# Kernel tuning notes

Measured on AMD Instinct MI355X. Metric: run time of the kernel, lower is better.

The kernel has to match this reference:

```python
import jax, jax.numpy as jnp
import numpy as np
import math

D_MODEL = 1024
NHEAD = 16
D_K = D_MODEL // NHEAD
B, S = 2, 2048


def setup_inputs() -> dict:
    key = jax.random.key(0)
    ks = jax.random.split(key, 9)
    x = jax.random.normal(ks[0], (B, S, D_MODEL), dtype=jnp.float32)
    # causal mask, broadcastable to (B, nhead, S, S); 0 entries are masked out
    mask = jnp.tril(jnp.ones((S, S), dtype=jnp.int32))[None, None, :, :]
    scale = 1.0 / math.sqrt(D_MODEL)
    def lin(kw, kb):
        W = jax.random.uniform(kw, (D_MODEL, D_MODEL), dtype=jnp.float32, minval=-scale, maxval=scale)
        b = jax.random.uniform(kb, (D_MODEL,), dtype=jnp.float32, minval=-scale, maxval=scale)
        return W, b
    Wq, bq = lin(ks[1], ks[2])
    Wk, bk = lin(ks[3], ks[4])
    Wv, bv = lin(ks[5], ks[6])
    Wo, bo = lin(ks[7], ks[8])
    return {"x": x, "mask": mask, "Wq": Wq, "bq": bq, "Wk": Wk, "bk": bk,
            "Wv": Wv, "bv": bv, "Wo": Wo, "bo": bo}


def reference(x, mask, Wq, bq, Wk, bk, Wv, bv, Wo, bo):
    b, s, _ = x.shape
    def heads(W, bias):
        # (b, s, d_model) @ (d_model, d_model) -> (b, nhead, s, d_k)
        return (x @ W.T + bias).reshape(b, s, NHEAD, D_K).transpose(0, 2, 1, 3)
    Q, K, V = heads(Wq, bq), heads(Wk, bk), heads(Wv, bv)
    scores = jnp.einsum('bhqd,bhkd->bhqk', Q, K) / math.sqrt(D_K)
    scores = jnp.where(mask == 0, jnp.float32(-1e9), scores)
    attn = jax.nn.softmax(scores, axis=-1)  # dropout is identity in eval mode
    out = jnp.einsum('bhqk,bhkd->bhqd', attn, V)
    out = out.transpose(0, 2, 1, 3).reshape(b, s, D_MODEL)
    return out @ Wo.T + bo
```

## Files before the change

### kernel.cpp

```cpp
#include <hip/hip_runtime.h>
#include <hip/hip_bf16.h>

#define DMODEL 1024
#define NH     16
#define DKH    64
#define BSZ    2
#define SEQ    2048
#define MROWS  (BSZ*SEQ)
#define WELEM  (DMODEL*DMODEL)

typedef __attribute__((ext_vector_type(8))) short short8;
typedef __attribute__((ext_vector_type(4))) short short4v;
typedef __attribute__((ext_vector_type(4))) float f32x4;

__device__ __forceinline__ f32x4 mfma_pv16(short4v a, short4v b, f32x4 c) {
#if defined(__HIP_DEVICE_COMPILE__)
#if __has_builtin(__builtin_amdgcn_mfma_f32_16x16x16bf16_1k)
    return __builtin_amdgcn_mfma_f32_16x16x16bf16_1k(a, b, c, 0, 0, 0);
#elif __has_builtin(__builtin_amdgcn_mfma_f32_16x16x16_bf16)
    return __builtin_amdgcn_mfma_f32_16x16x16_bf16(a, b, c, 0, 0, 0);
#else
    f32x4 d;
    asm volatile("v_mfma_f32_16x16x16_bf16 %0, %1, %2, %3"
                 : "=v"(d) : "v"(a), "v"(b), "v"(c));
    return d;
#endif
#else
    (void)a; (void)b;
    return c;
#endif
}

__device__ __forceinline__ ushort f2bf(float f) {
    return __bfloat16_as_ushort(__float2bfloat16(f));
}
__device__ __forceinline__ unsigned pk2(float lo, float hi) {
    return (unsigned)f2bf(lo) | ((unsigned)f2bf(hi) << 16);
}
__device__ __forceinline__ void load_lds16(const ushort* g, ushort* l) {
    __builtin_amdgcn_global_load_lds(
        (const __attribute__((address_space(1))) unsigned int*)g,
        (__attribute__((address_space(3))) unsigned int*)l, 16, 0, 0);
}

__global__ __launch_bounds__(256)
void cvt_all(const float* __restrict__ x,
             const float* __restrict__ W0, const float* __restrict__ W1,
             const float* __restrict__ W2, const float* __restrict__ W3,
             ushort* __restrict__ xbf, ushort* __restrict__ Wcat,
             ushort* __restrict__ Wo)
{
    const int blk = blockIdx.x;
    const float* src;
    ushort* dst;
    int base;
    if (blk < 2048)      { src = x;  dst = xbf;             base = blk * 2048; }
    else if (blk < 2560) { src = W0; dst = Wcat;            base = (blk - 2048) * 2048; }
    else if (blk < 3072) { src = W1; dst = Wcat + WELEM;    base = (blk - 2560) * 2048; }
    else if (blk < 3584) { src = W2; dst = Wcat + 2*WELEM;  base = (blk - 3072) * 2048; }
    else                 { src = W3; dst = Wo;              base = (blk - 3584) * 2048; }
    const size_t off = (size_t)base + threadIdx.x * 8;
    const float4 f0 = *(const float4*)(src + off);
    const float4 f1 = *(const float4*)(src + off + 4);
    uint4 o;
    o.x = pk2(f0.x, f0.y); o.y = pk2(f0.z, f0.w);
    o.z = pk2(f1.x, f1.y); o.w = pk2(f1.z, f1.w);
    *(uint4*)(dst + off) = o;
}

__global__ __launch_bounds__(256)
void gemm_qkv(const ushort* __restrict__ xbf, const ushort* __restrict__ Wcat,
              const float* __restrict__ bq, const float* __restrict__ bk,
              const float* __restrict__ bv,
              ushort* __restrict__ Qh, ushort* __restrict__ Kh,
              ushort* __restrict__ VT)
{
    __shared__ ushort Ash[128][32];
    __shared__ ushort Bsh[128][32];

    const int t    = threadIdx.x;
    const int m0   = blockIdx.y * 128, n0 = blockIdx.x * 128;
    const int wave = t >> 6;
    const int lane = t & 63;
    const int wr   = (wave >> 1) * 64;
    const int wc   = (wave & 1) * 64;
    const int quad = lane >> 4;
    const int r16  = lane & 15;

    const int row0 = wave * 16 + (lane >> 2);
    const int row1 = 64 + wave * 16 + (lane >> 2);
    const int ch   = (lane & 3) * 8;

    f32x4 acc[4][4];
    #pragma unroll
    for (int i = 0; i < 4; ++i)
        #pragma unroll
        for (int j = 0; j < 4; ++j)
            acc[i][j] = (f32x4){0.f, 0.f, 0.f, 0.f};

    for (int k0 = 0; k0 < DMODEL; k0 += 32) {
        load_lds16(xbf  + (size_t)(m0 + row0) * DMODEL + k0 + ch, &Ash[wave * 16][0]);
        load_lds16(xbf  + (size_t)(m0 + row1) * DMODEL + k0 + ch, &Ash[64 + wave * 16][0]);
        load_lds16(Wcat + (size_t)(n0 + row0) * DMODEL + k0 + ch, &Bsh[wave * 16][0]);
        load_lds16(Wcat + (size_t)(n0 + row1) * DMODEL + k0 + ch, &Bsh[64 + wave * 16][0]);
        __syncthreads();

        short8 af[4], bf[4];
        #pragma unroll
        for (int i = 0; i < 4; ++i) af[i] = *(const short8*)&Ash[wr + i * 16 + r16][quad * 8];
        #pragma unroll
        for (int j = 0; j < 4; ++j) bf[j] = *(const short8*)&Bsh[wc + j * 16 + r16][quad * 8];

        #pragma unroll
        for (int i = 0; i < 4; ++i)
            #pragma unroll
            for (int j = 0; j < 4; ++j)
                acc[i][j] = __builtin_amdgcn_mfma_f32_16x16x32_bf16(af[i], bf[j], acc[i][j], 0, 0, 0);
        __syncthreads();
    }

    const int region = n0 >> 10;
    const float* bp  = (region == 0) ? bq : (region == 1) ? bk : bv;
    ushort* outQK    = (region == 0) ? Qh : Kh;
    const float osc  = (region == 0) ? 0.18033688f : 1.0f;
    const int nbase  = n0 & 1023;

    #pragma unroll
    for (int i = 0; i < 4; ++i) {
        #pragma unroll
        for (int j = 0; j < 4; ++j) {
            #pragma unroll
            for (int reg = 0; reg < 4; ++reg) {
                const int m  = m0 + wr + i * 16 + quad * 4 + reg;
                const int n  = nbase + wc + j * 16 + r16;
                const float v = (acc[i][j][reg] + bp[n]) * osc;
                const int b = m >> 11, s = m & (SEQ - 1);
                const int h = n >> 6,  dk = n & 63;
                if (region < 2) {
                    outQK[((size_t)(b * NH + h) * SEQ + s) * DKH + dk] = f2bf(v);
                } else {
                    VT[(((size_t)(b * NH + h)) * DKH + dk) * SEQ + s] = f2bf(v);
                }
            }
        }
    }
}

__global__ __launch_bounds__(256)
void gemm_out(const ushort* __restrict__ O, const ushort* __restrict__ Wo,
              const float* __restrict__ bo, float* __restrict__ out)
{
    __shared__ ushort Ash[128][32];
    __shared__ ushort Bsh[64][32];

    const int t    = threadIdx.x;
    const int m0   = blockIdx.y * 128, n0 = blockIdx.x * 64;
    const int wave = t >> 6;
    const int lane = t & 63;
    const int wr   = (wave >> 1) * 64;
    const int wc   = (wave & 1) * 32;
    const int quad = lane >> 4;
    const int r16  = lane & 15;

    const int row0 = wave * 16 + (lane >> 2);
    const int row1 = 64 + wave * 16 + (lane >> 2);
    const int ch   = (lane & 3) * 8;

    f32x4 acc[4][2];
    #pragma unroll
    for (int i = 0; i < 4; ++i)
        #pragma unroll
        for (int j = 0; j < 2; ++j)
            acc[i][j] = (f32x4){0.f, 0.f, 0.f, 0.f};

    for (int k0 = 0; k0 < DMODEL; k0 += 32) {
        const int ma0 = m0 + row0, ma1 = m0 + row1;
        load_lds16(O + ((size_t)(ma0 >> 11) * NH + (k0 >> 6)) * (SEQ * DKH)
                     + (size_t)(ma0 & (SEQ - 1)) * DKH + (k0 & 63) + ch,
                   &Ash[wave * 16][0]);
        load_lds16(O + ((size_t)(ma1 >> 11) * NH + (k0 >> 6)) * (SEQ * DKH)
                     + (size_t)(ma1 & (SEQ - 1)) * DKH + (k0 & 63) + ch,
                   &Ash[64 + wave * 16][0]);
        load_lds16(Wo + (size_t)(n0 + row0) * DMODEL + k0 + ch, &Bsh[wave * 16][0]);
        __syncthreads();

        short8 af[4], bf[2];
        #pragma unroll
        for (int i = 0; i < 4; ++i) af[i] = *(const short8*)&Ash[wr + i * 16 + r16][quad * 8];
        #pragma unroll
        for (int j = 0; j < 2; ++j) bf[j] = *(const short8*)&Bsh[wc + j * 16 + r16][quad * 8];

        #pragma unroll
        for (int i = 0; i < 4; ++i)
            #pragma unroll
            for (int j = 0; j < 2; ++j)
                acc[i][j] = __builtin_amdgcn_mfma_f32_16x16x32_bf16(af[i], bf[j], acc[i][j], 0, 0, 0);
        __syncthreads();
    }

    #pragma unroll
    for (int i = 0; i < 4; ++i) {
        #pragma unroll
        for (int j = 0; j < 2; ++j) {
            #pragma unroll
            for (int reg = 0; reg < 4; ++reg) {
                const int m = m0 + wr + i * 16 + quad * 4 + reg;
                const int n = n0 + wc + j * 16 + r16;
                out[(size_t)m * DMODEL + n] = acc[i][j][reg] + bo[n];
            }
        }
    }
}

__global__ __launch_bounds__(256)
void gemm_mfma(const void* __restrict__ A, const void* __restrict__ W,
               const float* __restrict__ bias, void* __restrict__ out,
               int amode, int bmode, int outmode, float oscale)
{
    __shared__ ushort Ash[128][40];
    __shared__ ushort Bsh[128][40];

    const int t    = threadIdx.x;
    const int m0   = blockIdx.y * 128, n0 = blockIdx.x * 128;
    const int srow = t >> 1;
    const int shal = (t & 1) * 16;

    const int wave = t >> 6;
    const int lane = t & 63;
    const int wr   = (wave >> 1) * 64;
    const int wc   = (wave & 1) * 64;
    const int quad = lane >> 4;
    const int r16  = lane & 15;

    f32x4 acc[4][4];
    #pragma unroll
    for (int i = 0; i < 4; ++i)
        #pragma unroll
        for (int j = 0; j < 4; ++j)
            acc[i][j] = (f32x4){0.f, 0.f, 0.f, 0.f};

    for (int k0 = 0; k0 < DMODEL; k0 += 32) {
        uint4 a01, a23, b01, b23;
        if (amode == 0) {
            const float* ap = (const float*)A + (size_t)(m0 + srow) * DMODEL + k0 + shal;
            const float4 f0 = *(const float4*)(ap);
            const float4 f1 = *(const float4*)(ap + 4);
            const float4 f2 = *(const float4*)(ap + 8);
            const float4 f3 = *(const float4*)(ap + 12);
            a01 = (uint4){pk2(f0.x,f0.y), pk2(f0.z,f0.w), pk2(f1.x,f1.y), pk2(f1.z,f1.w)};
            a23 = (uint4){pk2(f2.x,f2.y), pk2(f2.z,f2.w), pk2(f3.x,f3.y), pk2(f3.z,f3.w)};
        } else if (amode == 1) {
            const int m = m0 + srow;
            const ushort* ap = (const ushort*)A
                + ((size_t)(m >> 11) * NH + (k0 >> 6)) * (SEQ * DKH)
                + (size_t)(m & (SEQ - 1)) * DKH + (k0 & 63) + shal;
            a01 = *(const uint4*)(ap);
            a23 = *(const uint4*)(ap + 8);
        } else {
            const ushort* ap = (const ushort*)A + (size_t)(m0 + srow) * DMODEL + k0 + shal;
            a01 = *(const uint4*)(ap);
            a23 = *(const uint4*)(ap + 8);
        }
        if (bmode == 0) {
            const float* wp = (const float*)W + (size_t)(n0 + srow) * DMODEL + k0 + shal;
            const float4 w0 = *(const float4*)(wp);
            const float4 w1 = *(const float4*)(wp + 4);
            const float4 w2 = *(const float4*)(wp + 8);
            const float4 w3 = *(const float4*)(wp + 12);
            b01 = (uint4){pk2(w0.x,w0.y), pk2(w0.z,w0.w), pk2(w1.x,w1.y), pk2(w1.z,w1.w)};
            b23 = (uint4){pk2(w2.x,w2.y), pk2(w2.z,w2.w), pk2(w3.x,w3.y), pk2(w3.z,w3.w)};
        } else {
            const ushort* wp = (const ushort*)W + (size_t)(n0 + srow) * DMODEL + k0 + shal;
            b01 = *(const uint4*)(wp);
            b23 = *(const uint4*)(wp + 8);
        }

        *(uint4*)&Ash[srow][shal]     = a01;
        *(uint4*)&Ash[srow][shal + 8] = a23;
        *(uint4*)&Bsh[srow][shal]     = b01;
        *(uint4*)&Bsh[srow][shal + 8] = b23;
        __syncthreads();

        short8 af[4], bf[4];
        #pragma unroll
        for (int i = 0; i < 4; ++i) af[i] = *(const short8*)&Ash[wr + i * 16 + r16][quad * 8];
        #pragma unroll
        for (int j = 0; j < 4; ++j) bf[j] = *(const short8*)&Bsh[wc + j * 16 + r16][quad * 8];

        #pragma unroll
        for (int i = 0; i < 4; ++i)
            #pragma unroll
            for (int j = 0; j < 4; ++j)
                acc[i][j] = __builtin_amdgcn_mfma_f32_16x16x32_bf16(af[i], bf[j], acc[i][j], 0, 0, 0);
        __syncthreads();
    }

    #pragma unroll
    for (int i = 0; i < 4; ++i) {
        #pragma unroll
        for (int j = 0; j < 4; ++j) {
            #pragma unroll
            for (int reg = 0; reg < 4; ++reg) {
                const int m = m0 + wr + i * 16 + quad * 4 + reg;
                const int n = n0 + wc + j * 16 + r16;
                const float v = (acc[i][j][reg] + bias[n]) * oscale;
                if (outmode == 0) {
                    ((float*)out)[(size_t)m * DMODEL + n] = v;
                } else if (outmode == 1) {
                    ((ushort*)out)[((size_t)(m >> 11) * NH + (n >> 6)) * (SEQ * DKH)
                                   + (size_t)(m & (SEQ - 1)) * DKH + (n & 63)] = f2bf(v);
                } else {
                    ((ushort*)out)[(((size_t)(m >> 11) * NH + (n >> 6)) * DKH + (n & 63)) * SEQ
                                   + (m & (SEQ - 1))] = f2bf(v);
                }
            }
        }
    }
}

__global__ __launch_bounds__(256, 3)
void attn_flash(ushort* __restrict__ Qh,
                const ushort* __restrict__ Kh,
                const ushort* __restrict__ VT)
{
    __shared__ ushort Kl[128][72];
    __shared__ ushort Vl[64][136];

    const int t256 = threadIdx.x;
    const int wave = t256 >> 6;
    const int lane = t256 & 63;
    const int quad = lane >> 4;
    const int r16  = lane & 15;

    const int slot = blockIdx.x & 7;
    const int bh   = slot * 4 + ((blockIdx.x >> 3) & 3);
    const int qt   = 15 - (blockIdx.x >> 5);
    const int q0   = qt * 128;

    ushort*       Qbase = Qh + (size_t)bh * SEQ * DKH;
    const ushort* Kbase = Kh + (size_t)bh * SEQ * DKH;
    const ushort* Vbase = VT + (size_t)bh * DKH * SEQ;

    short8 qf[2][2];
    #pragma unroll
    for (int g = 0; g < 2; ++g) {
        const ushort* qrow = Qbase + (size_t)(q0 + wave * 32 + g * 16 + r16) * DKH;
        qf[g][0] = *(const short8*)(qrow + quad * 8);
        qf[g][1] = *(const short8*)(qrow + 32 + quad * 8);
    }

    f32x4 oacc[2][4];
    #pragma unroll
    for (int g = 0; g < 2; ++g)
        #pragma unroll
        for (int i = 0; i < 4; ++i) oacc[g][i] = (f32x4){0.f, 0.f, 0.f, 0.f};
    f32x4 lsum4[2] = {(f32x4){0.f,0.f,0.f,0.f}, (f32x4){0.f,0.f,0.f,0.f}};

    const int T = qt + 1;

    const int krow = t256 >> 1, kc = (t256 & 1) * 32;
    const int vrow = t256 >> 2, vc = (t256 & 3) * 32;
    const ushort* kg0 = Kbase + (size_t)krow * DKH + kc;
    const ushort* vg0 = Vbase + (size_t)vrow * SEQ + vc;

    uint4 kr0, kr1, kr2, kr3, vr0, vr1, vr2, vr3;
    kr0 = *(const uint4*)(kg0);
    kr1 = *(const uint4*)(kg0 + 8);
    kr2 = *(const uint4*)(kg0 + 16);
    kr3 = *(const uint4*)(kg0 + 24);
    vr0 = *(const uint4*)(vg0);
    vr1 = *(const uint4*)(vg0 + 8);
    vr2 = *(const uint4*)(vg0 + 16);
    vr3 = *(const uint4*)(vg0 + 24);

    for (int t = 0; t < T - 1; ++t) {
        *(uint4*)&Kl[krow][kc]      = kr0;
        *(uint4*)&Kl[krow][kc + 8]  = kr1;
        *(uint4*)&Kl[krow][kc + 16] = kr2;
        *(uint4*)&Kl[krow][kc + 24] = kr3;
        *(uint4*)&Vl[vrow][vc]      = vr0;
        *(uint4*)&Vl[vrow][vc + 8]  = vr1;
        *(uint4*)&Vl[vrow][vc + 16] = vr2;
        *(uint4*)&Vl[vrow][vc + 24] = vr3;
        __syncthreads();

        {
            const ushort* kg = kg0 + (size_t)(t + 1) * 128 * DKH;
            kr0 = *(const uint4*)(kg);
            kr1 = *(const uint4*)(kg + 8);
            kr2 = *(const uint4*)(kg + 16);
            kr3 = *(const uint4*)(kg + 24);
            const ushort* vg = vg0 + (size_t)(t + 1) * 128;
            vr0 = *(const uint4*)(vg);
            vr1 = *(const uint4*)(vg + 8);
            vr2 = *(const uint4*)(vg + 16);
            vr3 = *(const uint4*)(vg + 24);
        }

        #pragma unroll
        for (int nt = 0; nt < 8; ++nt) {
            short8 b0 = *(const short8*)&Kl[nt * 16 + r16][quad * 8];
            short8 b1 = *(const short8*)&Kl[nt * 16 + r16][32 + quad * 8];
            short4v vb0 = *(const short4v*)&Vl[ 0 + r16][nt * 16 + quad * 4];
            short4v vb1 = *(const short4v*)&Vl[16 + r16][nt * 16 + quad * 4];
            short4v vb2 = *(const short4v*)&Vl[32 + r16][nt * 16 + quad * 4];
            short4v vb3 = *(const short4v*)&Vl[48 + r16][nt * 16 + quad * 4];

            #pragma unroll
            for (int g = 0; g < 2; ++g) {
                f32x4 s = (f32x4){0.f, 0.f, 0.f, 0.f};
                __builtin_amdgcn_s_setprio(1);
                s = __builtin_amdgcn_mfma_f32_16x16x32_bf16(b0, qf[g][0], s, 0, 0, 0);
                s = __builtin_amdgcn_mfma_f32_16x16x32_bf16(b1, qf[g][1], s, 0, 0, 0);
                __builtin_amdgcn_s_setprio(0);

                const float e0 = __builtin_amdgcn_exp2f(s[0]);
                const float e1 = __builtin_amdgcn_exp2f(s[1]);
                const float e2 = __builtin_amdgcn_exp2f(s[2]);
                const float e3 = __builtin_amdgcn_exp2f(s[3]);
                lsum4[g] += (f32x4){e0, e1, e2, e3};
                union { uint2 u; short4v s4; } pw;
                pw.u.x = pk2(e0, e1);
                pw.u.y = pk2(e2, e3);

                __builtin_amdgcn_s_setprio(1);
                oacc[g][0] = mfma_pv16(pw.s4, vb0, oacc[g][0]);
                oacc[g][1] = mfma_pv16(pw.s4, vb1, oacc[g][1]);
                oacc[g][2] = mfma_pv16(pw.s4, vb2, oacc[g][2]);
                oacc[g][3] = mfma_pv16(pw.s4, vb3, oacc[g][3]);
                __builtin_amdgcn_s_setprio(0);
            }
        }
        __syncthreads();
    }

    {
        *(uint4*)&Kl[krow][kc]      = kr0;
        *(uint4*)&Kl[krow][kc + 8]  = kr1;
        *(uint4*)&Kl[krow][kc + 16] = kr2;
        *(uint4*)&Kl[krow][kc + 24] = kr3;
        *(uint4*)&Vl[vrow][vc]      = vr0;
        *(uint4*)&Vl[vrow][vc + 8]  = vr1;
        *(uint4*)&Vl[vrow][vc + 16] = vr2;
        *(uint4*)&Vl[vrow][vc + 24] = vr3;
        __syncthreads();

        #pragma unroll
        for (int nt = 0; nt < 8; ++nt) {
            if (nt <= wave * 2 + 1) {
                short8 b0 = *(const short8*)&Kl[nt * 16 + r16][quad * 8];
                short8 b1 = *(const short8*)&Kl[nt * 16 + r16][32 + quad * 8];
                short4v vb0 = *(const short4v*)&Vl[ 0 + r16][nt * 16 + quad * 4];
                short4v vb1 = *(const short4v*)&Vl[16 + r16][nt * 16 + quad * 4];
                short4v vb2 = *(const short4v*)&Vl[32 + r16][nt * 16 + quad * 4];
                short4v vb3 = *(const short4v*)&Vl[48 + r16][nt * 16 + quad * 4];
                const int kbase = nt * 16 + quad * 4;

                #pragma unroll
                for (int g = 0; g < 2; ++g) {
                    if (nt <= wave * 2 + g) {
                        const int qrel = wave * 32 + g * 16 + r16;
                        f32x4 s = (f32x4){0.f, 0.f, 0.f, 0.f};
                        __builtin_amdgcn_s_setprio(1);
                        s = __builtin_amdgcn_mfma_f32_16x16x32_bf16(b0, qf[g][0], s, 0, 0, 0);
                        s = __builtin_amdgcn_mfma_f32_16x16x32_bf16(b1, qf[g][1], s, 0, 0, 0);
                        __builtin_amdgcn_s_setprio(0);

                        float e0 = __builtin_amdgcn_exp2f(s[0]);
                        float e1 = __builtin_amdgcn_exp2f(s[1]);
                        float e2 = __builtin_amdgcn_exp2f(s[2]);
                        float e3 = __builtin_amdgcn_exp2f(s[3]);
                        if (kbase + 0 > qrel) e0 = 0.f;
                        if (kbase + 1 > qrel) e1 = 0.f;
                        if (kbase + 2 > qrel) e2 = 0.f;
                        if (kbase + 3 > qrel) e3 = 0.f;
                        lsum4[g] += (f32x4){e0, e1, e2, e3};
                        union { uint2 u; short4v s4; } pw;
                        pw.u.x = pk2(e0, e1);
                        pw.u.y = pk2(e2, e3);

                        __builtin_amdgcn_s_setprio(1);
                        oacc[g][0] = mfma_pv16(pw.s4, vb0, oacc[g][0]);
                        oacc[g][1] = mfma_pv16(pw.s4, vb1, oacc[g][1]);
                        oacc[g][2] = mfma_pv16(pw.s4, vb2, oacc[g][2]);
                        oacc[g][3] = mfma_pv16(pw.s4, vb3, oacc[g][3]);
                        __builtin_amdgcn_s_setprio(0);
                    }
                }
            }
        }
    }

    #pragma unroll
    for (int g = 0; g < 2; ++g) {
        float lsum = (lsum4[g][0] + lsum4[g][1]) + (lsum4[g][2] + lsum4[g][3]);
        lsum += __shfl_xor(lsum, 16, 64);
        lsum += __shfl_xor(lsum, 32, 64);

        #pragma unroll
        for (int reg = 0; reg < 4; ++reg) {
            const float inv = 1.f / __shfl(lsum, quad * 4 + reg, 64);
            const int q = q0 + wave * 32 + g * 16 + quad * 4 + reg;
            ushort* orow = Qbase + (size_t)q * DKH;
            #pragma unroll
            for (int ct = 0; ct < 4; ++ct)
                orow[ct * 16 + r16] = f2bf(oacc[g][ct][reg] * inv);
        }
    }
}

extern "C" void kernel_launch(void* const* d_in, const int* in_sizes, int n_in,
                              void* d_out, int out_size, void* d_ws, size_t ws_size,
                              hipStream_t stream)
{
    const float* x  = (const float*)d_in[0];
    const float* Wf[4] = {(const float*)d_in[2], (const float*)d_in[4],
                          (const float*)d_in[6], (const float*)d_in[8]};
    const float* Bf[4] = {(const float*)d_in[3], (const float*)d_in[5],
                          (const float*)d_in[7], (const float*)d_in[9]};

    const size_t HSZ = (size_t)MROWS * DMODEL;
    ushort* Qh = (ushort*)d_ws;
    ushort* Kh = (ushort*)d_out;
    ushort* VT = (ushort*)d_out + HSZ;

    const dim3 blk(256);

    if (ws_size >= 24u * 1024 * 1024) {
        ushort* Wcat = Qh + HSZ;
        ushort* Wo   = Wcat + 3 * (size_t)WELEM;
        ushort* xbf  = Wo + WELEM;

        cvt_all<<<dim3(4096), blk, 0, stream>>>(x, Wf[0], Wf[1], Wf[2], Wf[3],
                                                xbf, Wcat, Wo);

        gemm_qkv<<<dim3(3 * DMODEL / 128, MROWS / 128), blk, 0, stream>>>(
            xbf, Wcat, Bf[0], Bf[1], Bf[2], Qh, Kh, VT);

        attn_flash<<<dim3(BSZ * NH * 16), dim3(256), 0, stream>>>(Qh, Kh, VT);

        gemm_out<<<dim3(DMODEL / 64, MROWS / 128), blk, 0, stream>>>(
            Qh, Wo, Bf[3], (float*)d_out);
    } else {
        const dim3 gg(DMODEL / 128, MROWS / 128);
        gemm_mfma<<<gg, blk, 0, stream>>>(x, Wf[0], Bf[0], Qh, 0, 0, 1, 0.18033688f);
        gemm_mfma<<<gg, blk, 0, stream>>>(x, Wf[1], Bf[1], Kh, 0, 0, 1, 1.0f);
        gemm_mfma<<<gg, blk, 0, stream>>>(x, Wf[2], Bf[2], VT, 0, 0, 2, 1.0f);
        attn_flash<<<dim3(BSZ * NH * 16), dim3(256), 0, stream>>>(Qh, Kh, VT);
        gemm_mfma<<<gg, blk, 0, stream>>>(Qh, Wf[3], Bf[3], d_out, 1, 0, 0, 1.0f);
    }
}
```

Measured before the change: 198.3 us.

## Double-buffer LDS tiles in QKV and output projection GEMMs

New measurement: 226.6 us. +14.3%, slower.

```diff
diff --git a/kernel.cpp b/kernel.cpp
--- a/kernel.cpp
+++ b/kernel.cpp
@@ -75,8 +75,8 @@
               ushort* __restrict__ Qh, ushort* __restrict__ Kh,
               ushort* __restrict__ VT)
 {
-    __shared__ ushort Ash[128][32];
-    __shared__ ushort Bsh[128][32];
+    __shared__ ushort Ash[2][128][32];
+    __shared__ ushort Bsh[2][128][32];
 
     const int t    = threadIdx.x;
     const int m0   = blockIdx.y * 128, n0 = blockIdx.x * 128;
@@ -91,6 +91,33 @@
     const int row1 = 64 + wave * 16 + (lane >> 2);
     const int ch   = (lane & 3) * 8;
 
+    const ushort* A0 = xbf  + (size_t)(m0 + row0) * DMODEL + ch;
+    const ushort* A1 = xbf  + (size_t)(m0 + row1) * DMODEL + ch;
+    const ushort* B0 = Wcat + (size_t)(n0 + row0) * DMODEL + ch;
+    const ushort* B1 = Wcat + (size_t)(n0 + row1) * DMODEL + ch;
+
+#define STAGE_QKV(buf, kk) do {                                   \
+    load_lds16(A0 + (kk), &Ash[buf][wave * 16][0]);               \
+    load_lds16(A1 + (kk), &Ash[buf][64 + wave * 16][0]);          \
+    load_lds16(B0 + (kk), &Bsh[buf][wave * 16][0]);               \
+    load_lds16(B1 + (kk), &Bsh[buf][64 + wave * 16][0]);          \
+} while (0)
+
+#define COMPUTE_QKV(buf) do {                                     \
+    short8 af[4], bfr[4];                                         \
+    _Pragma("unroll")                                             \
+    for (int i = 0; i < 4; ++i)                                   \
+        af[i] = *(const short8*)&Ash[buf][wr + i * 16 + r16][quad * 8];  \
+    _Pragma("unroll")                                             \
+    for (int j = 0; j < 4; ++j)                                   \
+        bfr[j] = *(const short8*)&Bsh[buf][wc + j * 16 + r16][quad * 8]; \
+    _Pragma("unroll")                                             \
+    for (int i = 0; i < 4; ++i)                                   \
+        _Pragma("unroll")                                         \
+        for (int j = 0; j < 4; ++j)                               \
+            acc[i][j] = __builtin_amdgcn_mfma_f32_16x16x32_bf16(af[i], bfr[j], acc[i][j], 0, 0, 0); \
+} while (0)
+
     f32x4 acc[4][4];
     #pragma unroll
     for (int i = 0; i < 4; ++i)
@@ -98,26 +125,19 @@
         for (int j = 0; j < 4; ++j)
             acc[i][j] = (f32x4){0.f, 0.f, 0.f, 0.f};
 
-    for (int k0 = 0; k0 < DMODEL; k0 += 32) {
-        load_lds16(xbf  + (size_t)(m0 + row0) * DMODEL + k0 + ch, &Ash[wave * 16][0]);
-        load_lds16(xbf  + (size_t)(m0 + row1) * DMODEL + k0 + ch, &Ash[64 + wave * 16][0]);
-        load_lds16(Wcat + (size_t)(n0 + row0) * DMODEL + k0 + ch, &Bsh[wave * 16][0]);
-        load_lds16(Wcat + (size_t)(n0 + row1) * DMODEL + k0 + ch, &Bsh[64 + wave * 16][0]);
-        __syncthreads();
-
-        short8 af[4], bf[4];
-        #pragma unroll
-        for (int i = 0; i < 4; ++i) af[i] = *(const short8*)&Ash[wr + i * 16 + r16][quad * 8];
-        #pragma unroll
-        for (int j = 0; j < 4; ++j) bf[j] = *(const short8*)&Bsh[wc + j * 16 + r16][quad * 8];
-
-        #pragma unroll
-        for (int i = 0; i < 4; ++i)
-            #pragma unroll
-            for (int j = 0; j < 4; ++j)
-                acc[i][j] = __builtin_amdgcn_mfma_f32_16x16x32_bf16(af[i], bf[j], acc[i][j], 0, 0, 0);
-        __syncthreads();
-    }
+    STAGE_QKV(0, 0);
+    __syncthreads();
+
+    for (int k0 = 0; k0 < DMODEL; k0 += 64) {
+        STAGE_QKV(1, k0 + 32);
+        COMPUTE_QKV(0);
+        __syncthreads();
+        if (k0 + 64 < DMODEL) STAGE_QKV(0, k0 + 64);
+        COMPUTE_QKV(1);
+        __syncthreads();
+    }
+#undef STAGE_QKV
+#undef COMPUTE_QKV
 
     const int region = n0 >> 10;
     const float* bp  = (region == 0) ? bq : (region == 1) ? bk : bv;
@@ -150,8 +170,8 @@
 void gemm_out(const ushort* __restrict__ O, const ushort* __restrict__ Wo,
               const float* __restrict__ bo, float* __restrict__ out)
 {
-    __shared__ ushort Ash[128][32];
-    __shared__ ushort Bsh[64][32];
+    __shared__ ushort Ash[2][128][32];
+    __shared__ ushort Bsh[2][64][32];
 
     const int t    = threadIdx.x;
     const int m0   = blockIdx.y * 128, n0 = blockIdx.x * 64;
@@ -165,6 +185,33 @@
     const int row0 = wave * 16 + (lane >> 2);
     const int row1 = 64 + wave * 16 + (lane >> 2);
     const int ch   = (lane & 3) * 8;
+    const int ma0  = m0 + row0, ma1 = m0 + row1;
+
+#define STAGE_OUT(buf, kk) do {                                               \
+    load_lds16(O + ((size_t)(ma0 >> 11) * NH + ((kk) >> 6)) * (SEQ * DKH)     \
+                 + (size_t)(ma0 & (SEQ - 1)) * DKH + ((kk) & 63) + ch,        \
+               &Ash[buf][wave * 16][0]);                                      \
+    load_lds16(O + ((size_t)(ma1 >> 11) * NH + ((kk) >> 6)) * (SEQ * DKH)     \
+                 + (size_t)(ma1 & (SEQ - 1)) * DKH + ((kk) & 63) + ch,        \
+               &Ash[buf][64 + wave * 16][0]);                                 \
+    load_lds16(Wo + (size_t)(n0 + row0) * DMODEL + (kk) + ch,                 \
+               &Bsh[buf][wave * 16][0]);                                      \
+} while (0)
+
+#define COMPUTE_OUT(buf) do {                                                 \
+    short8 af[4], bfr[2];                                                     \
+    _Pragma("unroll")                                                         \
+    for (int i = 0; i < 4; ++i)                                               \
+        af[i] = *(const short8*)&Ash[buf][wr + i * 16 + r16][quad * 8];       \
+    _Pragma("unroll")                                                         \
+    for (int j = 0; j < 2; ++j)                                               \
+        bfr[j] = *(const short8*)&Bsh[buf][wc + j * 16 + r16][quad * 8];      \
+    _Pragma("unroll")                                                         \
+    for (int i = 0; i < 4; ++i)                                               \
+        _Pragma("unroll")                                                     \
+        for (int j = 0; j < 2; ++j)                                           \
+            acc[i][j] = __builtin_amdgcn_mfma_f32_16x16x32_bf16(af[i], bfr[j], acc[i][j], 0, 0, 0); \
+} while (0)
 
     f32x4 acc[4][2];
     #pragma unroll
@@ -173,30 +220,19 @@
         for (int j = 0; j < 2; ++j)
             acc[i][j] = (f32x4){0.f, 0.f, 0.f, 0.f};
 
-    for (int k0 = 0; k0 < DMODEL; k0 += 32) {
-        const int ma0 = m0 + row0, ma1 = m0 + row1;
-        load_lds16(O + ((size_t)(ma0 >> 11) * NH + (k0 >> 6)) * (SEQ * DKH)
-                     + (size_t)(ma0 & (SEQ - 1)) * DKH + (k0 & 63) + ch,
-                   &Ash[wave * 16][0]);
-        load_lds16(O + ((size_t)(ma1 >> 11) * NH + (k0 >> 6)) * (SEQ * DKH)
-                     + (size_t)(ma1 & (SEQ - 1)) * DKH + (k0 & 63) + ch,
-                   &Ash[64 + wave * 16][0]);
-        load_lds16(Wo + (size_t)(n0 + row0) * DMODEL + k0 + ch, &Bsh[wave * 16][0]);
-        __syncthreads();
-
-        short8 af[4], bf[2];
-        #pragma unroll
-        for (int i = 0; i < 4; ++i) af[i] = *(const short8*)&Ash[wr + i * 16 + r16][quad * 8];
-        #pragma unroll
-        for (int j = 0; j < 2; ++j) bf[j] = *(const short8*)&Bsh[wc + j * 16 + r16][quad * 8];
-
-        #pragma unroll
-        for (int i = 0; i < 4; ++i)
-            #pragma unroll
-            for (int j = 0; j < 2; ++j)
-                acc[i][j] = __builtin_amdgcn_mfma_f32_16x16x32_bf16(af[i], bf[j], acc[i][j], 0, 0, 0);
-        __syncthreads();
-    }
+    STAGE_OUT(0, 0);
+    __syncthreads();
+
+    for (int k0 = 0; k0 < DMODEL; k0 += 64) {
+        STAGE_OUT(1, k0 + 32);
+        COMPUTE_OUT(0);
+        __syncthreads();
+        if (k0 + 64 < DMODEL) STAGE_OUT(0, k0 + 64);
+        COMPUTE_OUT(1);
+        __syncthreads();
+    }
+#undef STAGE_OUT
+#undef COMPUTE_OUT
 
     #pragma unroll
     for (int i = 0; i < 4; ++i) {
```
